# Kernel tuning notes

Measured on AMD Instinct MI355X. Metric: run time of the kernel, lower is better.

The kernel has to match this reference:

```python
import jax, jax.numpy as jnp
import numpy as np
from jax import lax

NPOINT = 512
RADIUS = 0.2
NSAMPLE = 32
BN_EPS = 1e-5


def farthest_point_sample(xyz, npoint):
    # xyz: [B, N, 3] -> centroids: [B, npoint] int32
    # Deterministic init (index 0) instead of torch's randint for reproducibility.
    B, N, _ = xyz.shape
    batch = jnp.arange(B)

    def body(carry, _):
        distance, farthest = carry
        centroid = xyz[batch, farthest][:, None, :]          # [B,1,3]
        dist = jnp.sum((xyz - centroid) ** 2, -1)             # [B,N]
        distance = jnp.minimum(distance, dist)
        new_far = jnp.argmax(distance, axis=-1).astype(jnp.int32)
        return (distance, new_far), farthest

    init = (jnp.full((B, N), 1e10, xyz.dtype), jnp.zeros((B,), jnp.int32))
    _, cents = lax.scan(body, init, None, length=npoint)      # [npoint, B]
    return cents.T


def gather_points(points, idx):
    # points: [B,N,C], idx: [B,...] -> [B,...,C]
    return jax.vmap(lambda p, i: p[i])(points, idx)


def query_ball_point(radius, nsample, xyz, new_xyz):
    # xyz: [B,N,3], new_xyz: [B,S,3] -> idx: [B,S,nsample]
    B, N, _ = xyz.shape
    sqrdists = jnp.sum((new_xyz[:, :, None, :] - xyz[:, None, :, :]) ** 2, -1)  # [B,S,N]
    gidx = jnp.where(sqrdists > radius * radius, N, jnp.arange(N))
    gidx = jnp.sort(gidx, axis=-1)[:, :, :nsample]
    first = gidx[:, :, :1]
    return jnp.where(gidx == N, first, gidx)


def setup_inputs() -> dict:
    key = jax.random.key(0)
    ks = jax.random.split(key, 8)
    B, N, D = 16, 8192, 3
    inp = {
        "xyz": jax.random.uniform(ks[0], (B, N, 3), jnp.float32),
        "points": jax.random.normal(ks[1], (B, N, D), jnp.float32),
    }
    chans = [D + 3, 64, 64, 128]
    for i in range(3):
        cin, cout = chans[i], chans[i + 1]
        inp[f"w{i}"] = jax.random.normal(ks[2 + i], (cout, cin), jnp.float32) / np.sqrt(cin)
        inp[f"b{i}"] = jnp.zeros((cout,), jnp.float32)
        inp[f"g{i}"] = jnp.ones((cout,), jnp.float32)
        inp[f"beta{i}"] = jnp.zeros((cout,), jnp.float32)
    return inp


def _forward(xyz, points, params):
    fps_idx = farthest_point_sample(xyz, NPOINT)               # [B,S]
    new_xyz = gather_points(xyz, fps_idx)                      # [B,S,3]
    idx = query_ball_point(RADIUS, NSAMPLE, xyz, new_xyz)      # [B,S,K]
    grouped_xyz = gather_points(xyz, idx) - new_xyz[:, :, None, :]  # [B,S,K,3]
    grouped_pts = gather_points(points, idx)                   # [B,S,K,D]
    feat = jnp.concatenate([grouped_xyz, grouped_pts], -1)     # [B,S,K,3+D]
    for w, b, g, be in params:
        feat = jnp.einsum('bskc,oc->bsko', feat, w) + b        # 1x1 conv
        mean = jnp.mean(feat, axis=(0, 1, 2))                  # BN (training stats)
        var = jnp.var(feat, axis=(0, 1, 2))
        feat = g * (feat - mean) * lax.rsqrt(var + BN_EPS) + be
        feat = jax.nn.relu(feat)
    new_points = jnp.max(feat, axis=2)                         # max over nsample -> [B,S,Cout]
    return new_xyz, new_points


def reference(xyz, points, w0, b0, g0, beta0, w1, b1, g1, beta1, w2, b2, g2, beta2):
    params = [(w0, b0, g0, beta0), (w1, b1, g1, beta1), (w2, b2, g2, beta2)]
    return _forward(xyz, points, params)
```

## Files before the change

kernel.cpp:

```cpp
#include <hip/hip_runtime.h>
#include <hip/hip_bf16.h>
#include <cstdint>
#include <cstddef>

#define NB 16
#define NN 8192
#define NS 512
#define NK 32
#define NG (NB*NS)
#define GPB 4
#define NBLK (NG/GPB)
#define NPOSI 262144

__device__ __forceinline__ double sq3d(double dx, double dy, double dz){
#pragma clang fp contract(off)
  const double a = dx*dx;
  const double b = dy*dy;
  const double c = dz*dz;
  return (a + b) + c;
}

template<int CTRL>
__device__ __forceinline__ unsigned dpp_umax_step(unsigned v){
  const unsigned o = (unsigned)__builtin_amdgcn_update_dpp(0, (int)v, CTRL, 0xf, 0xf, false);
  return v > o ? v : o;
}
__device__ __forceinline__ unsigned wave_umax63(unsigned v){
  v = dpp_umax_step<0xB1>(v);
  v = dpp_umax_step<0x4E>(v);
  v = dpp_umax_step<0x141>(v);
  v = dpp_umax_step<0x140>(v);
  v = dpp_umax_step<0x142>(v);
  v = dpp_umax_step<0x143>(v);
  return v;
}
__device__ __forceinline__ unsigned grp16_umax(unsigned v){
  v = dpp_umax_step<0xB1>(v);
  v = dpp_umax_step<0x4E>(v);
  v = dpp_umax_step<0x141>(v);
  v = dpp_umax_step<0x140>(v);
  return v;
}

__device__ __forceinline__ unsigned mort4(unsigned v){
  return (v & 1u) | ((v & 2u) << 2) | ((v & 4u) << 4) | ((v & 8u) << 6);
}

__global__ __launch_bounds__(1024) void k_morton(const float* __restrict__ xyz,
                                                 int* __restrict__ ord){
  const int b = blockIdx.x;
  const int t = threadIdx.x;
  const float* __restrict__ X = xyz + (size_t)b*NN*3;
  __shared__ unsigned sHist[4096];
  __shared__ unsigned sWT[16];
  for (int k=t; k<4096; k+=1024) sHist[k] = 0u;
  __syncthreads();
  unsigned code[8];
#pragma unroll
  for (int j=0;j<8;++j){
    const int p = t + 1024*j;
    const float x=X[p*3+0], y=X[p*3+1], z=X[p*3+2];
    const unsigned ix=(unsigned)min(15,max(0,(int)(x*16.f)));
    const unsigned iy=(unsigned)min(15,max(0,(int)(y*16.f)));
    const unsigned iz=(unsigned)min(15,max(0,(int)(z*16.f)));
    code[j] = mort4(ix) | (mort4(iy)<<1) | (mort4(iz)<<2);
    atomicAdd(&sHist[code[j]], 1u);
  }
  __syncthreads();
  {
    const uint4 h = ((const uint4*)sHist)[t];
    const unsigned l1=h.x, l2=h.x+h.y, l3=h.x+h.y+h.z, tot=l3+h.w;
    unsigned inc = tot;
    const int lane = t & 63;
#pragma unroll
    for (int d2=1; d2<64; d2<<=1){
      const unsigned v = __shfl_up(inc, d2);
      if (lane >= d2) inc += v;
    }
    const unsigned wexc = inc - tot;
    if (lane == 63) sWT[t>>6] = inc;
    __syncthreads();
    if (t == 0){
      unsigned run = 0;
#pragma unroll
      for (int k=0;k<16;++k){ const unsigned v=sWT[k]; sWT[k]=run; run+=v; }
    }
    __syncthreads();
    const unsigned base = sWT[t>>6] + wexc;
    uint4 o; o.x=base; o.y=base+l1; o.z=base+l2; o.w=base+l3;
    ((uint4*)sHist)[t] = o;
  }
  __syncthreads();
#pragma unroll
  for (int j=0;j<8;++j){
    const unsigned pos = atomicAdd(&sHist[code[j]], 1u);
    ord[(size_t)b*NN + pos] = t + 1024*j;
  }
}

__global__ __launch_bounds__(1024) void k_fps(const float* __restrict__ xyz,
                                              const int* __restrict__ ord,
                                              float* __restrict__ newxyz){
  const int b = blockIdx.x;
  const int t = threadIdx.x;
  const float* __restrict__ X = xyz + (size_t)b*NN*3;

  __shared__ float4 sP[NN];
  __shared__ unsigned long long sWv64[16];
  __shared__ int      sWi[16];
  __shared__ unsigned sWf[16];
  __shared__ unsigned sTag[16];
  __shared__ unsigned sF;
  __shared__ int sSel[NS];

  int oidx[8];
#pragma unroll
  for (int j=0;j<8;++j){
    const int p = t + 1024*j;
    sP[p] = make_float4(X[p*3+0], X[p*3+1], X[p*3+2], 0.f);
    oidx[j] = ord[(size_t)b*NN + 8*t + j];
  }
  if (t < 16) sTag[t] = 0u;
  if (t == 0) sF = 0u;
  __syncthreads();

  float px[8], py[8], pz[8], thr[8];
  double dd[8];
#pragma unroll
  for (int j=0;j<8;++j){
    const float4 q = sP[oidx[j]];
    px[j]=q.x; py[j]=q.y; pz[j]=q.z;
    dd[j]=1e10;
    thr[j]=fmaf(1e10f, 0x1p-19f, 1e10f);
  }
  float ctx=0.f, cty=0.f, ctz=0.f;
#pragma unroll
  for (int j=0;j<8;++j){ ctx+=px[j]; cty+=py[j]; ctz+=pz[j]; }
  ctx*=0.125f; cty*=0.125f; ctz*=0.125f;
  float r2m = 0.f;
#pragma unroll
  for (int j=0;j<8;++j){
    const float ax=px[j]-ctx, ay=py[j]-cty, az=pz[j]-ctz;
    r2m = fmaxf(r2m, fmaf(az,az,fmaf(ay,ay,ax*ax)));
  }
  const float rT = sqrtf(r2m)*(1.0f+0x1p-18f) + 0x1p-20f;

  double tmax = 1e10;
  float  tmax32 = 1e10f;
  int tio = oidx[0], ts = 0;
#pragma unroll
  for (int j=1;j<8;++j) if (oidx[j] < tio){ tio = oidx[j]; ts = j; }
  float skipgate = tmax32*(1.0f+0x1p-14f);

  int f = 0;
  const int lane = t & 63, wid = t >> 6;

  for (int i=0;i<NS;++i){
    if (t == 0) sSel[i] = f;
    if (i == NS-1) break;

    const float4 cf = sP[f];
    const float cx=cf.x, cy=cf.y, cz=cf.z;

    const float bx=cx-ctx, by=cy-cty, bz=cz-ctz;
    const float ddc = fmaf(bz,bz,fmaf(by,by,bx*bx));
    const float dcc = sqrtf(ddc);
    float s = dcc - rT; s = s - dcc*0x1p-16f;
    const bool engage = !(s > 0.f && s*s >= skipgate);

    if (engage){
      float e[8]; float mmin = 1e30f;
#pragma unroll
      for (int j=0;j<8;++j){
        const float ax=px[j]-cx, ay=py[j]-cy, az=pz[j]-cz;
        const float d32 = fmaf(az, az, fmaf(ay, ay, ax*ax));
        e[j] = d32 - thr[j];
        mmin = fminf(mmin, e[j]);
      }
      if (__builtin_expect(mmin <= 0.f, 0)){
        const double cxd=(double)cx, cyd=(double)cy, czd=(double)cz;
        bool needscan = false;
#pragma unroll
        for (int j=0;j<8;++j){
          if (e[j] <= 0.f){
            const double d64 = sq3d((double)px[j]-cxd, (double)py[j]-cyd, (double)pz[j]-czd);
            const double nd = fmin(dd[j], d64);
            needscan |= (j == ts) | (nd == tmax);
            dd[j] = nd;
            const float nd32 = (float)nd;
            thr[j] = fmaf(nd32, 0x1p-19f, nd32);
          }
        }
        if (needscan){
          double tm = dd[0]; int io = oidx[0]; int s0 = 0;
#pragma unroll
          for (int j=1;j<8;++j)
            if (dd[j] > tm || (dd[j] == tm && oidx[j] < io)){ tm=dd[j]; io=oidx[j]; s0=j; }
          tmax=tm; tio=io; ts=s0; tmax32=(float)tm;
          skipgate = tmax32*(1.0f+0x1p-14f);
        }
      }
    }

    const unsigned myb = __float_as_uint(tmax32);
    const unsigned wm = (unsigned)__builtin_amdgcn_readlane((int)wave_umax63(myb), 63);
    const unsigned long long mask = __ballot(myb == wm);
    int writer;
    if (__builtin_expect(__popcll(mask) == 1, 1)){
      writer = (int)__builtin_ctzll(mask);
    } else {
      double bestv = -1.0; int bestid = 0x7fffffff;
      unsigned long long mm = mask;
      while (mm){
        const int l = (int)__builtin_ctzll(mm);
        const double v = __shfl(tmax, l);
        const int   id = __shfl(tio, l);
        if (v > bestv || (v == bestv && id < bestid)){ bestv=v; bestid=id; }
        mm &= mm - 1;
      }
      writer = (int)__builtin_ctzll(__ballot(tmax == bestv && tio == bestid));
    }
    if (lane == writer){
      sWv64[wid] = (unsigned long long)__double_as_longlong(tmax);
      sWi[wid]   = tio;
      sWf[wid]   = wm;
      __hip_atomic_store(&sTag[wid], (unsigned)(i+1),
                         __ATOMIC_RELEASE, __HIP_MEMORY_SCOPE_WORKGROUP);
    }

    if (wid == 0){
      const int w = lane & 15;
      while (__hip_atomic_load(&sTag[w], __ATOMIC_ACQUIRE,
                               __HIP_MEMORY_SCOPE_WORKGROUP) != (unsigned)(i+1)) {}
      const double vb = __longlong_as_double((long long)sWv64[w]);
      const int    io = sWi[w];
      const unsigned wf = sWf[w];
      const unsigned m32 = grp16_umax(wf);
      const unsigned long long cm = __ballot(wf == m32) & 0xFFFFull;
      int fnew;
      if (__builtin_expect(__popcll(cm) == 1, 1)){
        fnew = __shfl(io, (int)__builtin_ctzll(cm));
      } else {
        double bestv = -1.0; int bestid = 0x7fffffff;
        unsigned long long mm = cm;
        while (mm){
          const int l = (int)__builtin_ctzll(mm);
          const double v = __shfl(vb, l);
          const int   id = __shfl(io, l);
          if (v > bestv || (v == bestv && id < bestid)){ bestv=v; bestid=id; }
          mm &= mm - 1;
        }
        fnew = bestid;
      }
      if (lane == 0)
        __hip_atomic_store(&sF, (((unsigned)(i+1))<<13) | (unsigned)fnew,
                           __ATOMIC_RELEASE, __HIP_MEMORY_SCOPE_WORKGROUP);
    }

    unsigned v;
    do {
      v = __hip_atomic_load(&sF, __ATOMIC_ACQUIRE, __HIP_MEMORY_SCOPE_WORKGROUP);
    } while ((v >> 13) != (unsigned)(i+1));
    f = (int)(v & 8191u);
  }
  __syncthreads();
  if (t < NS){
    const int id = sSel[t];
    const float4 cf = sP[id];
    float* o = newxyz + ((size_t)b*NS + t)*3;
    o[0]=cf.x; o[1]=cf.y; o[2]=cf.z;
  }
}

__global__ __launch_bounds__(256) void k_ball(const float* __restrict__ xyz,
                                              const float* __restrict__ newxyz,
                                              int* __restrict__ idx){
  const int w = (blockIdx.x << 2) + (threadIdx.x >> 6);
  const int lane = threadIdx.x & 63;
  const int b = w >> 9;
  const float* __restrict__ C = newxyz + (size_t)w*3;
  const float cxf=C[0], cyf=C[1], czf=C[2];
  const double cx=(double)cxf, cy=(double)cyf, cz=(double)czf;
  const float* __restrict__ X = xyz + (size_t)b*NN*3;
  int* __restrict__ out = idx + (size_t)w*NK;
  const double R2 = 0.2*0.2;
  const float r2lo = 0.04f*(1.0f - 0x1p-16f);
  const float r2hi = 0.04f*(1.0f + 0x1p-16f);
  int count = 0, first = 0;
  for (int base=0; base<NN && count<NK; base+=64){
    const int p = base + lane;
    const float ax=X[p*3+0]-cxf, ay=X[p*3+1]-cyf, az=X[p*3+2]-czf;
    const float d32 = fmaf(az, az, fmaf(ay, ay, ax*ax));
    bool q;
    if (d32 <= r2lo)      q = true;
    else if (d32 > r2hi)  q = false;
    else {
      const double d = sq3d((double)X[p*3+0]-cx, (double)X[p*3+1]-cy, (double)X[p*3+2]-cz);
      q = !(d > R2);
    }
    const unsigned long long m = __ballot(q);
    if (q){
      const int pos = count + __popcll(m & ((1ull<<lane)-1ull));
      if (pos < NK) out[pos] = p;
    }
    if (count == 0 && m) first = base + __builtin_ctzll(m);
    count += __popcll(m);
  }
  if (lane >= count && lane < NK) out[lane] = first;
}

__device__ __forceinline__ void stats_reduce(
    float v[4][8], float* __restrict__ sRed, int t, int tp, int tc, int blk,
    int chtot, int choff, bool domm,
    float* __restrict__ pS, float* __restrict__ pQ,
    float* __restrict__ mxp, float* __restrict__ mnp)
{
  __syncthreads();
  float S=0.f, Q=0.f;
  for (int m=0;m<4;++m){
#pragma unroll
    for (int i=0;i<8;++i) sRed[tp*68 + tc*8 + i] = v[m][i];
    __syncthreads();
    if (t < 64){
      float mxv = -3.402823466e38f, mnv = 3.402823466e38f;
#pragma unroll
      for (int j=0;j<32;++j){
        const float x = sRed[j*68 + t];
        S += x; Q += x*x;
        mxv = fmaxf(mxv,x); mnv = fminf(mnv,x);
      }
      if (domm){
        const int gg = blk*GPB + m;
        mxp[(size_t)gg*128 + choff + t] = mxv;
        mnp[(size_t)gg*128 + choff + t] = mnv;
      }
    }
    __syncthreads();
  }
  if (t < 64){
    pS[(size_t)blk*chtot + choff + t] = S;
    pQ[(size_t)blk*chtot + choff + t] = Q;
  }
}

__device__ __forceinline__ void mm64(const float* __restrict__ sXl,
                                     const float* __restrict__ sWl,
                                     int tp, int tc, float v[4][8]){
#pragma unroll 4
  for (int k=0;k<64;++k){
    float xv[4], wv[8];
#pragma unroll
    for (int m=0;m<4;++m) xv[m] = sXl[(tp+32*m)*65 + k];
#pragma unroll
    for (int i=0;i<8;++i) wv[i] = sWl[(tc*8+i)*65 + k];
#pragma unroll
    for (int m=0;m<4;++m)
#pragma unroll
      for (int i=0;i<8;++i) v[m][i] += xv[m]*wv[i];
  }
}

template<int DEPTH>
__global__ __launch_bounds__(256) void k_pass(
    const float* __restrict__ xyz, const float* __restrict__ points,
    const float* __restrict__ newxyz, const int* __restrict__ idx,
    const float* __restrict__ w0, const float* __restrict__ b0,
    const float* __restrict__ w1, const float* __restrict__ b1,
    const float* __restrict__ w2, const float* __restrict__ b2,
    const float* __restrict__ ac,
    float* __restrict__ pS, float* __restrict__ pQ,
    float* __restrict__ mxp, float* __restrict__ mnp)
{
  __shared__ float smem[(DEPTH>=1) ? 14784 : 2304];
  float* sX0 = smem;
  float* sW0 = smem + 1024;
  float* sV  = smem + 1600;
  float* sRed= smem;
  float* sB2 = smem + 2176;
  float* sW1 = smem + 2304;
  float* sX  = smem + 6464;

  const int t = threadIdx.x;
  const int blk = blockIdx.x;
  const int tc = t & 7, tp = t >> 3;

  for (int i=t;i<384;i+=256) sW0[(i/6)*9 + (i%6)] = w0[i];
  if (t < 64) sV[t] = b0[t];
  if constexpr (DEPTH >= 1){
    if (t < 64){ sV[64+t]=ac[t]; sV[128+t]=ac[64+t]; sV[192+t]=b1[t]; }
    for (int i=t;i<4096;i+=256) sW1[(i>>6)*65 + (i&63)] = w1[i];
  }
  if constexpr (DEPTH == 2){
    if (t < 64){ sV[256+t]=ac[128+t]; sV[320+t]=ac[192+t]; }
    if (t < 128) sB2[t] = b2[t];
  }

  {
    const int pos = t & 127;
    const int gg = blk*GPB + (pos >> 5);
    const int b  = gg >> 9;
    const int id = idx[gg*NK + (pos & 31)];
    if (t < 128){
      const float* __restrict__ P = xyz + ((size_t)b*NN + id)*3;
      const float* __restrict__ C = newxyz + (size_t)gg*3;
      sX0[pos*8+0] = P[0]-C[0];
      sX0[pos*8+1] = P[1]-C[1];
      sX0[pos*8+2] = P[2]-C[2];
    } else {
      const float* __restrict__ P = points + ((size_t)b*NN + id)*3;
      sX0[pos*8+3] = P[0];
      sX0[pos*8+4] = P[1];
      sX0[pos*8+5] = P[2];
    }
  }
  __syncthreads();

  float v[4][8];
#pragma unroll
  for (int m=0;m<4;++m){
    const int pos = tp + 32*m;
    float xr[6];
#pragma unroll
    for (int c=0;c<6;++c) xr[c] = sX0[pos*8+c];
#pragma unroll
    for (int i=0;i<8;++i){
      const int ch = tc*8+i;
      float acc = sV[ch];
#pragma unroll
      for (int c=0;c<6;++c) acc += sW0[ch*9+c]*xr[c];
      v[m][i] = acc;
    }
  }

  if constexpr (DEPTH == 0){
    stats_reduce(v, sRed, t, tp, tc, blk, 64, 0, false, pS, pQ, mxp, mnp);
    return;
  } else {
#pragma unroll
    for (int m=0;m<4;++m){
      const int pos = tp + 32*m;
#pragma unroll
      for (int i=0;i<8;++i){
        const int ch = tc*8+i;
        sX[pos*65+ch] = fmaxf(sV[64+ch]*v[m][i] + sV[128+ch], 0.f);
      }
    }
    __syncthreads();
#pragma unroll
    for (int m=0;m<4;++m)
#pragma unroll
      for (int i=0;i<8;++i) v[m][i] = sV[192 + tc*8 + i];
    mm64(sX, sW1, tp, tc, v);

    if constexpr (DEPTH == 1){
      stats_reduce(v, sRed, t, tp, tc, blk, 64, 0, false, pS, pQ, mxp, mnp);
      return;
    } else {
      __syncthreads();
#pragma unroll
      for (int m=0;m<4;++m){
        const int pos = tp + 32*m;
#pragma unroll
        for (int i=0;i<8;++i){
          const int ch = tc*8+i;
          sX[pos*65+ch] = fmaxf(sV[256+ch]*v[m][i] + sV[320+ch], 0.f);
        }
      }
      __syncthreads();
      for (int o=0;o<2;++o){
        for (int i=t;i<4096;i+=256) sW1[(i>>6)*65 + (i&63)] = w2[o*4096 + i];
        __syncthreads();
#pragma unroll
        for (int m=0;m<4;++m)
#pragma unroll
          for (int i=0;i<8;++i) v[m][i] = sB2[o*64 + tc*8 + i];
        mm64(sX, sW1, tp, tc, v);
        stats_reduce(v, sRed, t, tp, tc, blk, 128, o*64, true, pS, pQ, mxp, mnp);
      }
      return;
    }
  }
}

__global__ __launch_bounds__(1024) void k_stats(const float* __restrict__ pS, const float* __restrict__ pQ,
                                                const float* __restrict__ g, const float* __restrict__ beta,
                                                float* __restrict__ a, float* __restrict__ c, int CH){
  __shared__ float sS[1024], sQ[1024];
  const int t = threadIdx.x;
  const int ch = t & (CH-1);
  const int seg = t / CH;
  const int SEG = 1024 / CH;
  const int rows = NBLK / SEG;
  float S=0.f, Q=0.f;
  const int j0 = seg*rows;
#pragma unroll 4
  for (int r=0;r<rows;++r){
    const size_t o = (size_t)(j0+r)*CH + ch;
    S += pS[o]; Q += pQ[o];
  }
  sS[t]=S; sQ[t]=Q;
  __syncthreads();
  if (t < CH){
    float aS=0.f, aQ=0.f;
    for (int s2=0;s2<SEG;++s2){ aS += sS[s2*CH+ch]; aQ += sQ[s2*CH+ch]; }
    const float mean = aS * (1.f/(float)NPOSI);
    const float var  = fmaxf(aQ * (1.f/(float)NPOSI) - mean*mean, 0.f);
    const float av = g[ch] * rsqrtf(var + 1e-5f);
    a[ch] = av;
    c[ch] = beta[ch] - mean*av;
  }
}

__global__ __launch_bounds__(256) void k_final(const float* __restrict__ mxp, const float* __restrict__ mnp,
                                               const float* __restrict__ a, const float* __restrict__ c,
                                               float* __restrict__ out){
  const int i = blockIdx.x*256 + threadIdx.x;
  const int ch = i & 127;
  const float av = a[ch], cv = c[ch];
  const float vv = (av >= 0.f) ? mxp[i] : mnp[i];
  out[i] = fmaxf(av*vv + cv, 0.f);
}

extern "C" void kernel_launch(void* const* d_in, const int* in_sizes, int n_in,
                              void* d_out, int out_size, void* d_ws, size_t ws_size,
                              hipStream_t stream){
  (void)in_sizes; (void)n_in; (void)out_size;
  const float* xyz    = (const float*)d_in[0];
  const float* points = (const float*)d_in[1];
  const float* w0 = (const float*)d_in[2];
  const float* b0 = (const float*)d_in[3];
  const float* g0 = (const float*)d_in[4];
  const float* be0= (const float*)d_in[5];
  const float* w1 = (const float*)d_in[6];
  const float* b1 = (const float*)d_in[7];
  const float* g1 = (const float*)d_in[8];
  const float* be1= (const float*)d_in[9];
  const float* w2 = (const float*)d_in[10];
  const float* b2 = (const float*)d_in[11];
  const float* g2 = (const float*)d_in[12];
  const float* be2= (const float*)d_in[13];

  float* out_newxyz = (float*)d_out;
  float* out_newpts = out_newxyz + (size_t)NB*NS*3;

  char* ws = (char*)d_ws;
  int*   idx = (int*)ws;
  float* ac  = (float*)(ws + (1u<<20));
  float* pS  = (float*)(ws + (1u<<20) + 4096);
  float* pQ  = pS + (size_t)NBLK*128;
  float* mxp = pQ + (size_t)NBLK*128;
  float* mnp = mxp + (size_t)NG*128;
  const size_t need = (1u<<20) + 4096 + (size_t)2*NBLK*128*4 + (size_t)2*NG*128*4;
  if (ws_size < need) return;

  int* ord = idx;

  k_morton<<<NB, 1024, 0, stream>>>(xyz, ord);
  k_fps  <<<NB, 1024, 0, stream>>>(xyz, ord, out_newxyz);
  k_ball <<<NG/4, 256, 0, stream>>>(xyz, out_newxyz, idx);

  k_pass<0><<<NBLK,256,0,stream>>>(xyz,points,out_newxyz,idx,w0,b0,w1,b1,w2,b2,ac,pS,pQ,mxp,mnp);
  k_stats<<<1,1024,0,stream>>>(pS,pQ,g0,be0, ac+0,   ac+64,  64);
  k_pass<1><<<NBLK,256,0,stream>>>(xyz,points,out_newxyz,idx,w0,b0,w1,b1,w2,b2,ac,pS,pQ,mxp,mnp);
  k_stats<<<1,1024,0,stream>>>(pS,pQ,g1,be1, ac+128, ac+192, 64);
  k_pass<2><<<NBLK,256,0,stream>>>(xyz,points,out_newxyz,idx,w0,b0,w1,b1,w2,b2,ac,pS,pQ,mxp,mnp);
  k_stats<<<1,1024,0,stream>>>(pS,pQ,g2,be2, ac+256, ac+384, 128);
  k_final<<<(NG*128)/256,256,0,stream>>>(mxp,mnp,ac+256,ac+384,out_newpts);
}
```

Before: 1.162 ms.

## Replace two-stage FPS reduction with all-waves redundant cross-wave argmax

In the farthest-point-sampling kernel, each wave now publishes a single packed 64-bit word (key, iteration tag, index) into a double-buffered shared slot. Every wave polls all 16 slots and computes the block-wide winner itself, rather than waiting for wave 0 to reduce and broadcast through a second flag. This removes one serialized publish/acquire round trip per iteration. Centroid coordinates are written straight to global memory inside the loop instead of in a final pass. The cost is redundant reduction work in every wave and more LDS polling traffic, and correctness relies on the double-buffering parity to avoid overwrite races.

```diff
diff --git a/kernel.cpp b/kernel.cpp
--- a/kernel.cpp
+++ b/kernel.cpp
@@ -106,12 +106,8 @@
   const float* __restrict__ X = xyz + (size_t)b*NN*3;
 
   __shared__ float4 sP[NN];
-  __shared__ unsigned long long sWv64[16];
-  __shared__ int      sWi[16];
-  __shared__ unsigned sWf[16];
-  __shared__ unsigned sTag[16];
-  __shared__ unsigned sF;
-  __shared__ int sSel[NS];
+  __shared__ unsigned long long sW0[2][16];
+  __shared__ unsigned long long sWv64[2][16];
 
   int oidx[8];
 #pragma unroll
@@ -120,8 +116,7 @@
     sP[p] = make_float4(X[p*3+0], X[p*3+1], X[p*3+2], 0.f);
     oidx[j] = ord[(size_t)b*NN + 8*t + j];
   }
-  if (t < 16) sTag[t] = 0u;
-  if (t == 0) sF = 0u;
+  if (t < 16){ sW0[0][t]=0ull; sW0[1][t]=0ull; }
   __syncthreads();
 
   float px[8], py[8], pz[8], thr[8];
@@ -155,12 +150,14 @@
   int f = 0;
   const int lane = t & 63, wid = t >> 6;
 
-  for (int i=0;i<NS;++i){
-    if (t == 0) sSel[i] = f;
-    if (i == NS-1) break;
-
+  for (int i=0;i<NS-1;++i){
+    const int par = i & 1;
     const float4 cf = sP[f];
     const float cx=cf.x, cy=cf.y, cz=cf.z;
+    if (t == 0){
+      float* o = newxyz + ((size_t)b*NS + i)*3;
+      o[0]=cx; o[1]=cy; o[2]=cz;
+    }
 
     const float bx=cx-ctx, by=cy-cty, bz=cz-ctz;
     const float ddc = fmaf(bz,bz,fmaf(by,by,bx*bx));
@@ -221,53 +218,44 @@
       writer = (int)__builtin_ctzll(__ballot(tmax == bestv && tio == bestid));
     }
     if (lane == writer){
-      sWv64[wid] = (unsigned long long)__double_as_longlong(tmax);
-      sWi[wid]   = tio;
-      sWf[wid]   = wm;
-      __hip_atomic_store(&sTag[wid], (unsigned)(i+1),
+      sWv64[par][wid] = (unsigned long long)__double_as_longlong(tmax);
+      const unsigned long long pk = ((unsigned long long)wm << 32)
+                                  | ((unsigned long long)(unsigned)(i+1) << 13)
+                                  | (unsigned long long)(unsigned)tio;
+      __hip_atomic_store(&sW0[par][wid], pk,
                          __ATOMIC_RELEASE, __HIP_MEMORY_SCOPE_WORKGROUP);
     }
 
-    if (wid == 0){
-      const int w = lane & 15;
-      while (__hip_atomic_load(&sTag[w], __ATOMIC_ACQUIRE,
-                               __HIP_MEMORY_SCOPE_WORKGROUP) != (unsigned)(i+1)) {}
-      const double vb = __longlong_as_double((long long)sWv64[w]);
-      const int    io = sWi[w];
-      const unsigned wf = sWf[w];
-      const unsigned m32 = grp16_umax(wf);
-      const unsigned long long cm = __ballot(wf == m32) & 0xFFFFull;
-      int fnew;
-      if (__builtin_expect(__popcll(cm) == 1, 1)){
-        fnew = __shfl(io, (int)__builtin_ctzll(cm));
-      } else {
-        double bestv = -1.0; int bestid = 0x7fffffff;
-        unsigned long long mm = cm;
-        while (mm){
-          const int l = (int)__builtin_ctzll(mm);
-          const double v = __shfl(vb, l);
-          const int   id = __shfl(io, l);
-          if (v > bestv || (v == bestv && id < bestid)){ bestv=v; bestid=id; }
-          mm &= mm - 1;
-        }
-        fnew = bestid;
-      }
-      if (lane == 0)
-        __hip_atomic_store(&sF, (((unsigned)(i+1))<<13) | (unsigned)fnew,
-                           __ATOMIC_RELEASE, __HIP_MEMORY_SCOPE_WORKGROUP);
-    }
-
-    unsigned v;
+    const unsigned want = (unsigned)(i+1);
+    unsigned long long w;
     do {
-      v = __hip_atomic_load(&sF, __ATOMIC_ACQUIRE, __HIP_MEMORY_SCOPE_WORKGROUP);
-    } while ((v >> 13) != (unsigned)(i+1));
-    f = (int)(v & 8191u);
-  }
-  __syncthreads();
-  if (t < NS){
-    const int id = sSel[t];
-    const float4 cf = sP[id];
-    float* o = newxyz + ((size_t)b*NS + t)*3;
+      w = __hip_atomic_load(&sW0[par][lane & 15],
+                            __ATOMIC_RELAXED, __HIP_MEMORY_SCOPE_WORKGROUP);
+    } while (__ballot((((unsigned)w >> 13) & 1023u) == want) != ~0ull);
+    __builtin_amdgcn_fence(__ATOMIC_ACQUIRE, "workgroup");
+
+    const unsigned wf   = (unsigned)(w >> 32);
+    const unsigned idxw = (unsigned)w & 8191u;
+    const unsigned m32  = grp16_umax(wf);
+    const unsigned long long cm = __ballot(wf == m32);
+    if (__builtin_expect(__popcll(cm) == 4, 1)){
+      f = __shfl((int)idxw, (int)__builtin_ctzll(cm));
+    } else {
+      unsigned long long mm = cm & 0xFFFFull;
+      double bv = -1.0; int bid = 0x7fffffff;
+      while (mm){
+        const int l = (int)__builtin_ctzll(mm);
+        const double v = __longlong_as_double((long long)sWv64[par][l]);
+        const int   id = __shfl((int)idxw, l);
+        if (v > bv || (v == bv && id < bid)){ bv = v; bid = id; }
+        mm &= mm - 1;
+      }
+      f = bid;
+    }
+  }
+  if (t == 0){
+    const float4 cf = sP[f];
+    float* o = newxyz + ((size_t)b*NS + (NS-1))*3;
     o[0]=cf.x; o[1]=cf.y; o[2]=cf.z;
   }
 }
```

Result: faster. 1.079 ms (-7.1%).
